# Optimization experiments

Hardware: AMD Instinct MI355X
Metric: run time of the kernel (lower is better)

Reference implementation:

```python
import jax, jax.numpy as jnp
import numpy as np

D_MODEL = 1024
N_HEADS = 16
D_HEAD = D_MODEL // N_HEADS  # 64
NEG_INF = -1e10


def setup_inputs() -> dict:
    key = jax.random.key(0)
    ks = jax.random.split(key, 12)
    B, Q, N = 2, 2048, 2048
    s = 1.0 / np.sqrt(D_MODEL)
    return {
        "q": jax.random.normal(ks[0], (B, Q, D_MODEL), jnp.float32),
        "k": jax.random.normal(ks[1], (B, N, D_MODEL), jnp.float32),
        "v": jax.random.normal(ks[2], (B, N, D_MODEL), jnp.float32),
        "mask": jax.random.randint(ks[3], (B, Q, N), 0, 2, jnp.int32),
        "Wq": jax.random.normal(ks[4], (D_MODEL, D_MODEL), jnp.float32) * s,
        "bq": jnp.zeros((D_MODEL,), jnp.float32),
        "Wk": jax.random.normal(ks[5], (D_MODEL, D_MODEL), jnp.float32) * s,
        "bk": jnp.zeros((D_MODEL,), jnp.float32),
        "Wv": jax.random.normal(ks[6], (D_MODEL, D_MODEL), jnp.float32) * s,
        "bv": jnp.zeros((D_MODEL,), jnp.float32),
        "Wo": jax.random.normal(ks[7], (D_MODEL, D_MODEL), jnp.float32) * s,
        "bo": jnp.zeros((D_MODEL,), jnp.float32),
    }


def reference(q, k, v, mask, Wq, bq, Wk, bk, Wv, bv, Wo, bo):
    B, Qlen, _ = q.shape
    N = k.shape[1]
    scale = 1.0 / np.sqrt(D_HEAD).astype(np.float32)
    # projections -> [B, S, H, Dh]
    qp = (q @ Wq + bq).reshape(B, Qlen, N_HEADS, D_HEAD)
    kp = (k @ Wk + bk).reshape(B, N, N_HEADS, D_HEAD)
    vp = (v @ Wv + bv).reshape(B, N, N_HEADS, D_HEAD)
    # scores [B, H, Q, N]
    score = jnp.einsum('bqhi,bnhi->bhqn', qp, kp) * scale
    score = jnp.where(mask[:, None, :, :] == 0, NEG_INF, score)
    attn_w = jax.nn.softmax(score, axis=-1)
    # dropout p=0.0 -> identity
    attn_out = jnp.einsum('bhqn,bnhi->bqhi', attn_w, vp).reshape(B, Qlen, D_MODEL)
    out = attn_out @ Wo + bo
    return out, attn_w
```

## Files before the change

### kernel.cpp

```cpp
#include <hip/hip_runtime.h>
#include <hip/hip_bf16.h>

#define BB 2
#define SS 2048
#define DMODEL 1024
#define NH 16
#define DHEAD 64
#define NEGINF (-1e10f)

typedef __attribute__((ext_vector_type(8))) short short8;
typedef __attribute__((ext_vector_type(4))) short short4v;
typedef __attribute__((ext_vector_type(4))) float f32x4;
typedef __hip_bfloat16 bf16;

__device__ __forceinline__ bf16 tobf(float x){ return __float2bfloat16(x); }
__device__ __forceinline__ float tof(bf16 x){ return __bfloat162float(x); }

__device__ __forceinline__ void gl_lds16(const void* g, void* l){
  __builtin_amdgcn_global_load_lds(
      (const __attribute__((address_space(1))) unsigned int*)g,
      (__attribute__((address_space(3))) unsigned int*)l, 16, 0, 0);
}


__global__ __launch_bounds__(256) void k_a3(const float* __restrict__ X, bf16* __restrict__ X3){
  long i = ((long)blockIdx.x*256 + threadIdx.x)*4;
  long r = i >> 10; int k = (int)(i & 1023);
  float4 x = *(const float4*)(X + i);
  float xs[4] = {x.x, x.y, x.z, x.w};
  alignas(8) bf16 hb[4], lb[4];
  #pragma unroll
  for(int j=0;j<4;j++){ hb[j]=tobf(xs[j]); lb[j]=tobf(xs[j]-tof(hb[j])); }
  bf16* base = X3 + r*3072 + k;
  *(short4v*)(base)        = *(short4v*)hb;
  *(short4v*)(base + 1024) = *(short4v*)lb;
  *(short4v*)(base + 2048) = *(short4v*)hb;
}

__global__ __launch_bounds__(256) void k_vbf(const float* __restrict__ X, bf16* __restrict__ Y){
  long i = ((long)blockIdx.x*256 + threadIdx.x)*4;
  float4 x = *(const float4*)(X + i);
  alignas(8) bf16 b[4] = {tobf(x.x), tobf(x.y), tobf(x.z), tobf(x.w)};
  *(short4v*)(Y + i) = *(short4v*)b;
}

template<int MODE>
__global__ __launch_bounds__(256) void k_wt(const float* __restrict__ W, bf16* __restrict__ out){
  __shared__ float t[64][65];
  const int kb = blockIdx.y*64, nb = blockIdx.x*64;
  const int tid = threadIdx.x;
  const int r = tid>>2, cq = tid&3;
  #pragma unroll
  for(int i=0;i<4;i++){
    float4 x = *(const float4*)&W[(long)(kb+r)*1024 + nb + cq*16 + i*4];
    t[r][cq*16+i*4+0]=x.x; t[r][cq*16+i*4+1]=x.y; t[r][cq*16+i*4+2]=x.z; t[r][cq*16+i*4+3]=x.w;
  }
  __syncthreads();
  alignas(16) bf16 hb[16], lb[16];
  #pragma unroll
  for(int i=0;i<16;i++){
    float x = t[cq*16+i][r];
    hb[i] = tobf(x);
    lb[i] = tobf(x - tof(hb[i]));
  }
  if (MODE==0){
    bf16* o = out + (long)(nb+r)*1024 + kb + cq*16;
    ((short8*)o)[0] = ((short8*)hb)[0]; ((short8*)o)[1] = ((short8*)hb)[1];
  } else {
    bf16* o = out + (long)(nb+r)*3072 + kb + cq*16;
    ((short8*)(o))[0]        = ((short8*)hb)[0]; ((short8*)(o))[1]        = ((short8*)hb)[1];
    ((short8*)(o+1024))[0]   = ((short8*)hb)[0]; ((short8*)(o+1024))[1]   = ((short8*)hb)[1];
    ((short8*)(o+2048))[0]   = ((short8*)lb)[0]; ((short8*)(o+2048))[1]   = ((short8*)lb)[1];
  }
}

__global__ __launch_bounds__(256) void k_vt(const bf16* __restrict__ vp, bf16* __restrict__ vpt){
  __shared__ alignas(16) bf16 t[64][72];
  const int sb = blockIdx.x*64;
  const int bh = blockIdx.y, b = bh>>4, h = bh&15;
  const int tid = threadIdx.x;
  {
    const int r = tid>>2, cg = tid&3;
    const bf16* src = vp + (long)(b*SS + sb + r)*DMODEL + h*64 + cg*16;
    *(short8*)&t[r][cg*16]   = *(const short8*)(src);
    *(short8*)&t[r][cg*16+8] = *(const short8*)(src+8);
  }
  __syncthreads();
  {
    const int d = tid>>2, sg = tid&3;
    alignas(16) bf16 ob[16];
    #pragma unroll
    for(int i=0;i<16;i++) ob[i] = t[sg*16+i][d];
    bf16* dst = vpt + ((long)bh*DHEAD + d)*SS + sb + sg*16;
    ((short8*)dst)[0] = ((short8*)ob)[0]; ((short8*)dst)[1] = ((short8*)ob)[1];
  }
}

enum { EPI_F32BIAS=0, EPI_BF16=1, EPI_SCORES=2, EPI_SPL3A=3, EPI_SPL3B=4 };

template<int EPI>
__global__ __launch_bounds__(256)
void gemm128(const bf16* __restrict__ A, int lda, long sAz,
             const bf16* __restrict__ Bt, int ldb, long sBz,
             float* __restrict__ Cf, bf16* __restrict__ Cb,
             int ldc, long sCz,
             const float* __restrict__ bias,
             const int* __restrict__ mask,
             float scale, int K)
{
  __shared__ alignas(16) bf16 lds[2][2][128*32];
  const int tid = threadIdx.x, wid = tid>>6, lane = tid&63;
  const int wr = wid>>1, wc = wid&1;
  const long bz = blockIdx.z;
  const int rowB = blockIdx.y*128, colB = blockIdx.x*128;
  const bf16* Ab = A + bz*sAz;
  const bf16* Bb = Bt + bz*sBz;

  auto stage = [&](int buf, int kt){
    #pragma unroll
    for(int i=0;i<2;i++){
      const int r0 = wid*32 + i*16;
      const char* ga = (const char*)(Ab + (long)(rowB + r0 + (lane>>2))*lda + kt*32) + (lane&3)*16;
      gl_lds16(ga, (char*)&lds[buf][0][0] + r0*64);
      const char* gb = (const char*)(Bb + (long)(colB + r0 + (lane>>2))*ldb + kt*32) + (lane&3)*16;
      gl_lds16(gb, (char*)&lds[buf][1][0] + r0*64);
    }
  };

  f32x4 acc[4][4];
  #pragma unroll
  for(int m=0;m<4;m++){
    #pragma unroll
    for(int n=0;n<4;n++){ acc[m][n][0]=0.f; acc[m][n][1]=0.f; acc[m][n][2]=0.f; acc[m][n][3]=0.f; }
  }

  const int nk = K/32;
  stage(0,0);
  int cur=0;
  for(int kt=0; kt<nk; ++kt){
    __syncthreads();
    if (kt+1<nk) stage(cur^1, kt+1);
    const bf16* la = &lds[cur][0][0];
    const bf16* lb = &lds[cur][1][0];
    const int rr = lane&15, kq = (lane>>4)*8;
    short8 af[4], bg[4];
    #pragma unroll
    for(int m=0;m<4;m++) af[m] = *(const short8*)(la + (wr*64+m*16+rr)*32 + kq);
    #pragma unroll
    for(int n=0;n<4;n++) bg[n] = *(const short8*)(lb + (wc*64+n*16+rr)*32 + kq);
    #pragma unroll
    for(int m=0;m<4;m++){
      #pragma unroll
      for(int n=0;n<4;n++)
        acc[m][n] = __builtin_amdgcn_mfma_f32_16x16x32_bf16(af[m], bg[n], acc[m][n], 0,0,0);
    }
    cur ^= 1;
  }

  #pragma unroll
  for(int m=0;m<4;m++){
    #pragma unroll
    for(int n=0;n<4;n++){
      const int row0 = rowB + wr*64 + m*16 + ((lane>>4)<<2);
      const int col  = colB + wc*64 + n*16 + (lane&15);
      #pragma unroll
      for(int j=0;j<4;j++){
        const int row = row0 + j;
        float x = acc[m][n][j];
        if constexpr (EPI==EPI_F32BIAS){
          Cf[bz*sCz + (long)row*ldc + col] = x + bias[col];
        } else if constexpr (EPI==EPI_BF16){
          Cb[bz*sCz + (long)row*ldc + col] = tobf(x + bias[col]);
        } else if constexpr (EPI==EPI_SCORES){
          const int b = (int)(bz>>4);
          const float s = x*scale;
          const int mv = mask[((long)b*SS + row)*SS + col];
          Cf[bz*sCz + (long)row*ldc + col] = (mv==0) ? NEGINF : s;
        } else {
          const float s = x + bias[col];
          const int b = row>>11, sq = row&2047;
          const int h = col>>6,  d  = col&63;
          bf16 hi = tobf(s);
          bf16 lo = tobf(s - tof(hi));
          bf16* o = Cb + (((long)(b*NH+h)*SS + sq)*192);
          if constexpr (EPI==EPI_SPL3A){ o[d]=hi; o[64+d]=lo; o[128+d]=hi; }
          else                          { o[d]=hi; o[64+d]=hi; o[128+d]=lo; }
        }
      }
    }
  }
}

__global__ __launch_bounds__(256)
void gemm_pv(const float* __restrict__ P, const bf16* __restrict__ Vt, bf16* __restrict__ O)
{
  __shared__ alignas(16) bf16 lA[2][128*32];
  __shared__ alignas(16) bf16 lB[2][64*32];
  const int tid=threadIdx.x, wid=tid>>6, lane=tid&63;
  const long z = blockIdx.z;
  const int b = (int)(z>>4), h = (int)(z&15);
  const int rowB = blockIdx.y*128;
  const float* Pz = P + z*((long)SS*SS) + (long)rowB*SS;
  const bf16*  Vz = Vt + z*((long)DHEAD*SS);

  auto stageB = [&](int buf, int kt){
    const char* g = (const char*)(Vz + (long)(wid*16 + (lane>>2))*SS + kt*32) + (lane&3)*16;
    gl_lds16(g, (char*)&lB[buf][0] + wid*16*64);
  };
  const int ar = tid>>1, acg = tid&1;
  auto loadA = [&](int kt, float4* f){
    const float* src = Pz + (long)ar*SS + kt*32 + acg*16;
    #pragma unroll
    for(int i=0;i<4;i++) f[i] = *(const float4*)(src + i*4);
  };
  auto writeA = [&](int buf, const float4* f){
    alignas(16) bf16 tmp[16];
    #pragma unroll
    for(int i=0;i<4;i++){
      tmp[i*4+0]=tobf(f[i].x); tmp[i*4+1]=tobf(f[i].y);
      tmp[i*4+2]=tobf(f[i].z); tmp[i*4+3]=tobf(f[i].w);
    }
    short8* d = (short8*)(&lA[buf][ar*32 + acg*16]);
    d[0] = ((short8*)tmp)[0]; d[1] = ((short8*)tmp)[1];
  };

  f32x4 acc[2][4];
  #pragma unroll
  for(int m=0;m<2;m++){
    #pragma unroll
    for(int n=0;n<4;n++){ acc[m][n][0]=0.f; acc[m][n][1]=0.f; acc[m][n][2]=0.f; acc[m][n][3]=0.f; }
  }

  float4 fr[4];
  loadA(0, fr); stageB(0,0); writeA(0, fr);
  int cur=0;
  const int nk = SS/32;
  for(int kt=0; kt<nk; ++kt){
    __syncthreads();
    float4 fn[4];
    if (kt+1<nk){ stageB(cur^1, kt+1); loadA(kt+1, fn); }
    const int rr=lane&15, kq=(lane>>4)*8;
    short8 af[2], bg[4];
    #pragma unroll
    for(int m=0;m<2;m++) af[m] = *(const short8*)(&lA[cur][(wid*32+m*16+rr)*32 + kq]);
    #pragma unroll
    for(int n=0;n<4;n++) bg[n] = *(const short8*)(&lB[cur][(n*16+rr)*32 + kq]);
    #pragma unroll
    for(int m=0;m<2;m++){
      #pragma unroll
      for(int n=0;n<4;n++)
        acc[m][n] = __builtin_amdgcn_mfma_f32_16x16x32_bf16(af[m], bg[n], acc[m][n], 0,0,0);
    }
    if (kt+1<nk) writeA(cur^1, fn);
    cur ^= 1;
  }

  #pragma unroll
  for(int m=0;m<2;m++){
    #pragma unroll
    for(int n=0;n<4;n++){
      const int row0 = rowB + wid*32 + m*16 + ((lane>>4)<<2);
      const int col  = n*16 + (lane&15);
      #pragma unroll
      for(int j=0;j<4;j++){
        const int row = row0 + j;
        O[((long)(b*SS + row))*DMODEL + h*64 + col] = tobf(acc[m][n][j]);
      }
    }
  }
}

__global__ __launch_bounds__(256) void k_softmax(float* __restrict__ attn){
  const long row = (long)blockIdx.x*4 + (threadIdx.x>>6);
  const int lane = threadIdx.x & 63;
  float* p = attn + row*SS;
  float v[32];
  float mx = -3.0e38f;
  #pragma unroll
  for(int i=0;i<8;i++){
    float4 t = *(const float4*)(p + i*256 + lane*4);
    v[i*4+0]=t.x; v[i*4+1]=t.y; v[i*4+2]=t.z; v[i*4+3]=t.w;
    mx = fmaxf(mx, fmaxf(fmaxf(t.x,t.y), fmaxf(t.z,t.w)));
  }
  #pragma unroll
  for(int off=32; off; off>>=1) mx = fmaxf(mx, __shfl_xor(mx, off));
  float sum = 0.f;
  #pragma unroll
  for(int i=0;i<32;i++){ v[i] = __expf(v[i]-mx); sum += v[i]; }
  #pragma unroll
  for(int off=32; off; off>>=1) sum += __shfl_xor(sum, off);
  const float inv = 1.0f/sum;
  #pragma unroll
  for(int i=0;i<8;i++){
    float4 t = { v[i*4+0]*inv, v[i*4+1]*inv, v[i*4+2]*inv, v[i*4+3]*inv };
    *(float4*)(p + i*256 + lane*4) = t;
  }
}

extern "C" void kernel_launch(void* const* d_in, const int* in_sizes, int n_in,
                              void* d_out, int out_size, void* d_ws, size_t ws_size,
                              hipStream_t stream) {
  const float* q    = (const float*)d_in[0];
  const float* k    = (const float*)d_in[1];
  const float* v    = (const float*)d_in[2];
  const int*   mask = (const int*)  d_in[3];
  const float* Wq   = (const float*)d_in[4];
  const float* bq   = (const float*)d_in[5];
  const float* Wk   = (const float*)d_in[6];
  const float* bk   = (const float*)d_in[7];
  const float* Wv   = (const float*)d_in[8];
  const float* bv   = (const float*)d_in[9];
  const float* Wo   = (const float*)d_in[10];
  const float* bo   = (const float*)d_in[11];

  float* out  = (float*)d_out;
  float* attn = out + (long)BB*SS*DMODEL;

  char* ws = (char*)d_ws;
  size_t o = 0;
  bf16* A3q = (bf16*)(ws+o); o += (size_t)4096*3072*2;
  bf16* A3k = (bf16*)(ws+o); o += (size_t)4096*3072*2;
  bf16* vbf = (bf16*)(ws+o); o += (size_t)4096*1024*2;
  bf16* Wq3 = (bf16*)(ws+o); o += (size_t)1024*3072*2;
  bf16* Wk3 = (bf16*)(ws+o); o += (size_t)1024*3072*2;
  bf16* Wvt = (bf16*)(ws+o); o += (size_t)1024*1024*2;
  bf16* Wot = (bf16*)(ws+o); o += (size_t)1024*1024*2;
  bf16* q3  = (bf16*)(ws+o); o += (size_t)32*2048*192*2;
  bf16* k3  = (bf16*)(ws+o); o += (size_t)32*2048*192*2;
  bf16* vpb = (bf16*)(ws+o); o += (size_t)4096*1024*2;
  bf16* vpt = (bf16*)(ws+o); o += (size_t)32*64*2048*2;
  bf16* abf = (bf16*)(ws+o); o += (size_t)4096*1024*2;

  dim3 blk(256);
  k_a3 <<<4096, blk, 0, stream>>>(q, A3q);
  k_a3 <<<4096, blk, 0, stream>>>(k, A3k);
  k_vbf<<<4096, blk, 0, stream>>>(v, vbf);
  k_wt<1><<<dim3(16,16), blk, 0, stream>>>(Wq, Wq3);
  k_wt<1><<<dim3(16,16), blk, 0, stream>>>(Wk, Wk3);
  k_wt<0><<<dim3(16,16), blk, 0, stream>>>(Wv, Wvt);
  k_wt<0><<<dim3(16,16), blk, 0, stream>>>(Wo, Wot);
  gemm128<EPI_SPL3A><<<dim3(8,32,1), blk, 0, stream>>>(A3q,3072,0, Wq3,3072,0, nullptr,q3, 0,0, bq, nullptr, 0.f, 3072);
  gemm128<EPI_SPL3B><<<dim3(8,32,1), blk, 0, stream>>>(A3k,3072,0, Wk3,3072,0, nullptr,k3, 0,0, bk, nullptr, 0.f, 3072);
  gemm128<EPI_BF16 ><<<dim3(8,32,1), blk, 0, stream>>>(vbf,1024,0, Wvt,1024,0, nullptr,vpb, 1024,0, bv, nullptr, 0.f, 1024);
  k_vt<<<dim3(32,32), blk, 0, stream>>>(vpb, vpt);
  gemm128<EPI_SCORES><<<dim3(16,16,32), blk, 0, stream>>>(
      q3,192,(long)SS*192, k3,192,(long)SS*192, attn,nullptr, SS,(long)SS*SS,
      nullptr, mask, 0.125f, 192);
  k_softmax<<<(BB*NH*SS)/4, blk, 0, stream>>>(attn);
  gemm_pv<<<dim3(1,16,32), blk, 0, stream>>>(attn, vpt, abf);
  gemm128<EPI_F32BIAS><<<dim3(8,32,1), blk, 0, stream>>>(abf,1024,0, Wot,1024,0, out,nullptr, 1024,0, bo, nullptr, 0.f, 1024);
}
```

Baseline: 1.284 ms.

## Fuse softmax into scores and PV kernels with fp16 scores and bitpacked mask

```diff
diff --git a/kernel.cpp b/kernel.cpp
--- a/kernel.cpp
+++ b/kernel.cpp
@@ -1,5 +1,6 @@
 #include <hip/hip_runtime.h>
 #include <hip/hip_bf16.h>
+#include <hip/hip_fp16.h>
 
 #define BB 2
 #define SS 2048
@@ -7,6 +8,7 @@
 #define NH 16
 #define DHEAD 64
 #define NEGINF (-1e10f)
+#define MASKF16 (-65504.0f)
 
 typedef __attribute__((ext_vector_type(8))) short short8;
 typedef __attribute__((ext_vector_type(4))) short short4v;
@@ -22,6 +24,14 @@
       (__attribute__((address_space(3))) unsigned int*)l, 16, 0, 0);
 }
 
+
+__global__ __launch_bounds__(256) void k_maskbits(const int* __restrict__ mask,
+                                                  unsigned long long* __restrict__ bits){
+  long t = (long)blockIdx.x*256 + threadIdx.x;
+  int m = mask[t];
+  unsigned long long bal = __ballot(m != 0);
+  if ((threadIdx.x & 63) == 0) bits[t>>6] = bal;
+}
 
 __global__ __launch_bounds__(256) void k_a3(const float* __restrict__ X, bf16* __restrict__ X3){
   long i = ((long)blockIdx.x*256 + threadIdx.x)*4;
@@ -96,7 +106,7 @@
   }
 }
 
-enum { EPI_F32BIAS=0, EPI_BF16=1, EPI_SCORES=2, EPI_SPL3A=3, EPI_SPL3B=4 };
+enum { EPI_F32BIAS=0, EPI_BF16=1, EPI_SPL3A=3, EPI_SPL3B=4 };
 
 template<int EPI>
 __global__ __launch_bounds__(256)
@@ -105,8 +115,7 @@
              float* __restrict__ Cf, bf16* __restrict__ Cb,
              int ldc, long sCz,
              const float* __restrict__ bias,
-             const int* __restrict__ mask,
-             float scale, int K)
+             int K)
 {
   __shared__ alignas(16) bf16 lds[2][2][128*32];
   const int tid = threadIdx.x, wid = tid>>6, lane = tid&63;
@@ -171,11 +180,6 @@
           Cf[bz*sCz + (long)row*ldc + col] = x + bias[col];
         } else if constexpr (EPI==EPI_BF16){
           Cb[bz*sCz + (long)row*ldc + col] = tobf(x + bias[col]);
-        } else if constexpr (EPI==EPI_SCORES){
-          const int b = (int)(bz>>4);
-          const float s = x*scale;
-          const int mv = mask[((long)b*SS + row)*SS + col];
-          Cf[bz*sCz + (long)row*ldc + col] = (mv==0) ? NEGINF : s;
         } else {
           const float s = x + bias[col];
           const int b = row>>11, sq = row&2047;
@@ -192,7 +196,114 @@
 }
 
 __global__ __launch_bounds__(256)
-void gemm_pv(const float* __restrict__ P, const bf16* __restrict__ Vt, bf16* __restrict__ O)
+void gemm_scores(const bf16* __restrict__ A, const bf16* __restrict__ Bt,
+                 const unsigned int* __restrict__ bits,
+                 __half* __restrict__ Sf, float2* __restrict__ partials, float scale)
+{
+  __shared__ alignas(16) bf16 lds[2][2][128*32];
+  __shared__ unsigned int bitlds[128][4];
+  const int tid = threadIdx.x, wid = tid>>6, lane = tid&63;
+  const int wr = wid>>1, wc = wid&1;
+  const long z = blockIdx.z;
+  const int b = (int)(z>>4);
+  const int rowB = blockIdx.y*128, colB = blockIdx.x*128;
+  const bf16* Ab = A + z*((long)SS*192);
+  const bf16* Bb = Bt + z*((long)SS*192);
+
+  auto stage = [&](int buf, int kt){
+    #pragma unroll
+    for(int i=0;i<2;i++){
+      const int r0 = wid*32 + i*16;
+      const char* ga = (const char*)(Ab + (long)(rowB + r0 + (lane>>2))*192 + kt*32) + (lane&3)*16;
+      gl_lds16(ga, (char*)&lds[buf][0][0] + r0*64);
+      const char* gb = (const char*)(Bb + (long)(colB + r0 + (lane>>2))*192 + kt*32) + (lane&3)*16;
+      gl_lds16(gb, (char*)&lds[buf][1][0] + r0*64);
+    }
+  };
+
+  f32x4 acc[4][4];
+  #pragma unroll
+  for(int m=0;m<4;m++){
+    #pragma unroll
+    for(int n=0;n<4;n++){ acc[m][n][0]=0.f; acc[m][n][1]=0.f; acc[m][n][2]=0.f; acc[m][n][3]=0.f; }
+  }
+
+  stage(0,0);
+  int cur=0;
+  for(int kt=0; kt<6; ++kt){
+    __syncthreads();
+    if (kt+1<6) stage(cur^1, kt+1);
+    const bf16* la = &lds[cur][0][0];
+    const bf16* lb = &lds[cur][1][0];
+    const int rr = lane&15, kq = (lane>>4)*8;
+    short8 af[4], bg[4];
+    #pragma unroll
+    for(int m=0;m<4;m++) af[m] = *(const short8*)(la + (wr*64+m*16+rr)*32 + kq);
+    #pragma unroll
+    for(int n=0;n<4;n++) bg[n] = *(const short8*)(lb + (wc*64+n*16+rr)*32 + kq);
+    #pragma unroll
+    for(int m=0;m<4;m++){
+      #pragma unroll
+      for(int n=0;n<4;n++)
+        acc[m][n] = __builtin_amdgcn_mfma_f32_16x16x32_bf16(af[m], bg[n], acc[m][n], 0,0,0);
+    }
+    cur ^= 1;
+  }
+
+  if (tid < 128){
+    *(uint4*)&bitlds[tid][0] =
+        *(const uint4*)(bits + ((long)(b*SS + rowB + tid))*64 + (colB>>5));
+  }
+  __syncthreads();
+
+  __half* Sz = Sf + z*((long)SS*SS);
+  #pragma unroll
+  for(int m=0;m<4;m++){
+    #pragma unroll
+    for(int j=0;j<4;j++){
+      const int row_l = wr*64 + m*16 + ((lane>>4)<<2) + j;
+      const long rowOff = (long)(rowB + row_l)*SS;
+      float x[4];
+      #pragma unroll
+      for(int n=0;n<4;n++){
+        const int col_l = wc*64 + n*16 + (lane&15);
+        const unsigned w = bitlds[row_l][col_l>>5];
+        const bool keep = (w >> (col_l&31)) & 1u;
+        const float s = keep ? acc[m][n][j]*scale : MASKF16;
+        const __half hh = __float2half(s);
+        Sz[rowOff + colB + col_l] = hh;
+        x[n] = __half2float(hh);
+      }
+      float mx = fmaxf(fmaxf(x[0],x[1]), fmaxf(x[2],x[3]));
+      #pragma unroll
+      for(int off=1; off<16; off<<=1) mx = fmaxf(mx, __shfl_xor(mx, off));
+      float sm = __expf(x[0]-mx)+__expf(x[1]-mx)+__expf(x[2]-mx)+__expf(x[3]-mx);
+      #pragma unroll
+      for(int off=1; off<16; off<<=1) sm += __shfl_xor(sm, off);
+      if ((lane&15)==0)
+        partials[((long)z*SS + rowB + row_l)*32 + blockIdx.x*2 + wc] = make_float2(mx, sm);
+    }
+  }
+}
+
+__global__ __launch_bounds__(256) void k_stats(const float2* __restrict__ partials,
+                                               float2* __restrict__ stats){
+  const long row = (long)blockIdx.x*4 + (threadIdx.x>>6);
+  const int lane = threadIdx.x & 63;
+  float2 pr = make_float2(-3.0e38f, 0.f);
+  if (lane < 32) pr = partials[row*32 + lane];
+  float M = pr.x;
+  #pragma unroll
+  for(int off=32; off; off>>=1) M = fmaxf(M, __shfl_xor(M, off));
+  float v = (lane < 32) ? pr.y * __expf(pr.x - M) : 0.f;
+  #pragma unroll
+  for(int off=32; off; off>>=1) v += __shfl_xor(v, off);
+  if (lane == 0) stats[row] = make_float2(M, 1.0f / v);
+}
+
+__global__ __launch_bounds__(256)
+void gemm_pv(const __half* __restrict__ S, const float2* __restrict__ stats,
+             const bf16* __restrict__ Vt, float* __restrict__ attnw, bf16* __restrict__ O)
 {
   __shared__ alignas(16) bf16 lA[2][128*32];
   __shared__ alignas(16) bf16 lB[2][64*32];
@@ -200,7 +311,8 @@
   const long z = blockIdx.z;
   const int b = (int)(z>>4), h = (int)(z&15);
   const int rowB = blockIdx.y*128;
-  const float* Pz = P + z*((long)SS*SS) + (long)rowB*SS;
+  const __half* Sz = S + z*((long)SS*SS) + (long)rowB*SS;
+  float*       Wz = attnw + z*((long)SS*SS) + (long)rowB*SS;
   const bf16*  Vz = Vt + z*((long)DHEAD*SS);
 
   auto stageB = [&](int buf, int kt){
@@ -208,18 +320,24 @@
     gl_lds16(g, (char*)&lB[buf][0] + wid*16*64);
   };
   const int ar = tid>>1, acg = tid&1;
-  auto loadA = [&](int kt, float4* f){
-    const float* src = Pz + (long)ar*SS + kt*32 + acg*16;
-    #pragma unroll
-    for(int i=0;i<4;i++) f[i] = *(const float4*)(src + i*4);
+  const float2 st = stats[z*SS + rowB + ar];
+  const float M = st.x, invZ = st.y;
+
+  auto loadA = [&](int kt, short8* r){
+    const short8* src = (const short8*)(Sz + (long)ar*SS + kt*32 + acg*16);
+    r[0] = src[0]; r[1] = src[1];
   };
-  auto writeA = [&](int buf, const float4* f){
+  auto procA = [&](int buf, int kt, const short8* r){
+    const __half* hp = (const __half*)r;
+    alignas(16) float p[16];
+    #pragma unroll
+    for(int i=0;i<16;i++) p[i] = __expf(__half2float(hp[i]) - M) * invZ;
+    float* w = Wz + (long)ar*SS + kt*32 + acg*16;
+    #pragma unroll
+    for(int i=0;i<4;i++) *(float4*)(w + i*4) = *(float4*)&p[i*4];
     alignas(16) bf16 tmp[16];
     #pragma unroll
-    for(int i=0;i<4;i++){
-      tmp[i*4+0]=tobf(f[i].x); tmp[i*4+1]=tobf(f[i].y);
-      tmp[i*4+2]=tobf(f[i].z); tmp[i*4+3]=tobf(f[i].w);
-    }
+    for(int i=0;i<16;i++) tmp[i] = tobf(p[i]);
     short8* d = (short8*)(&lA[buf][ar*32 + acg*16]);
     d[0] = ((short8*)tmp)[0]; d[1] = ((short8*)tmp)[1];
   };
@@ -231,13 +349,13 @@
     for(int n=0;n<4;n++){ acc[m][n][0]=0.f; acc[m][n][1]=0.f; acc[m][n][2]=0.f; acc[m][n][3]=0.f; }
   }
 
-  float4 fr[4];
-  loadA(0, fr); stageB(0,0); writeA(0, fr);
+  short8 fr[2];
+  loadA(0, fr); stageB(0,0); procA(0, 0, fr);
   int cur=0;
   const int nk = SS/32;
   for(int kt=0; kt<nk; ++kt){
     __syncthreads();
-    float4 fn[4];
+    short8 fn[2];
     if (kt+1<nk){ stageB(cur^1, kt+1); loadA(kt+1, fn); }
     const int rr=lane&15, kq=(lane>>4)*8;
     short8 af[2], bg[4];
@@ -251,7 +369,7 @@
       for(int n=0;n<4;n++)
         acc[m][n] = __builtin_amdgcn_mfma_f32_16x16x32_bf16(af[m], bg[n], acc[m][n], 0,0,0);
     }
-    if (kt+1<nk) writeA(cur^1, fn);
+    if (kt+1<nk) procA(cur^1, kt+1, fn);
     cur ^= 1;
   }
 
@@ -267,33 +385,6 @@
         O[((long)(b*SS + row))*DMODEL + h*64 + col] = tobf(acc[m][n][j]);
       }
     }
-  }
-}
-
-__global__ __launch_bounds__(256) void k_softmax(float* __restrict__ attn){
-  const long row = (long)blockIdx.x*4 + (threadIdx.x>>6);
-  const int lane = threadIdx.x & 63;
-  float* p = attn + row*SS;
-  float v[32];
-  float mx = -3.0e38f;
-  #pragma unroll
-  for(int i=0;i<8;i++){
-    float4 t = *(const float4*)(p + i*256 + lane*4);
-    v[i*4+0]=t.x; v[i*4+1]=t.y; v[i*4+2]=t.z; v[i*4+3]=t.w;
-    mx = fmaxf(mx, fmaxf(fmaxf(t.x,t.y), fmaxf(t.z,t.w)));
-  }
-  #pragma unroll
-  for(int off=32; off; off>>=1) mx = fmaxf(mx, __shfl_xor(mx, off));
-  float sum = 0.f;
-  #pragma unroll
-  for(int i=0;i<32;i++){ v[i] = __expf(v[i]-mx); sum += v[i]; }
-  #pragma unroll
-  for(int off=32; off; off>>=1) sum += __shfl_xor(sum, off);
-  const float inv = 1.0f/sum;
-  #pragma unroll
-  for(int i=0;i<8;i++){
-    float4 t = { v[i*4+0]*inv, v[i*4+1]*inv, v[i*4+2]*inv, v[i*4+3]*inv };
-    *(float4*)(p + i*256 + lane*4) = t;
   }
 }
 
@@ -330,8 +421,13 @@
   bf16* vpb = (bf16*)(ws+o); o += (size_t)4096*1024*2;
   bf16* vpt = (bf16*)(ws+o); o += (size_t)32*64*2048*2;
   bf16* abf = (bf16*)(ws+o); o += (size_t)4096*1024*2;
+  unsigned long long* bits = (unsigned long long*)(ws+o); o += (size_t)BB*SS*32*8;
+  __half* scoresF = (__half*)(ws+o); o += (size_t)32*SS*SS*2;
+  float2* partials = (float2*)(ws+o); o += (size_t)32*SS*32*8;
+  float2* stats   = (float2*)(ws+o); o += (size_t)32*SS*8;
 
   dim3 blk(256);
+  k_maskbits<<<(BB*SS*SS)/256, blk, 0, stream>>>(mask, bits);
   k_a3 <<<4096, blk, 0, stream>>>(q, A3q);
   k_a3 <<<4096, blk, 0, stream>>>(k, A3k);
   k_vbf<<<4096, blk, 0, stream>>>(v, vbf);
@@ -339,14 +435,13 @@
   k_wt<1><<<dim3(16,16), blk, 0, stream>>>(Wk, Wk3);
   k_wt<0><<<dim3(16,16), blk, 0, stream>>>(Wv, Wvt);
   k_wt<0><<<dim3(16,16), blk, 0, stream>>>(Wo, Wot);
-  gemm128<EPI_SPL3A><<<dim3(8,32,1), blk, 0, stream>>>(A3q,3072,0, Wq3,3072,0, nullptr,q3, 0,0, bq, nullptr, 0.f, 3072);
-  gemm128<EPI_SPL3B><<<dim3(8,32,1), blk, 0, stream>>>(A3k,3072,0, Wk3,3072,0, nullptr,k3, 0,0, bk, nullptr, 0.f, 3072);
-  gemm128<EPI_BF16 ><<<dim3(8,32,1), blk, 0, stream>>>(vbf,1024,0, Wvt,1024,0, nullptr,vpb, 1024,0, bv, nullptr, 0.f, 1024);
+  gemm128<EPI_SPL3A><<<dim3(8,32,1), blk, 0, stream>>>(A3q,3072,0, Wq3,3072,0, nullptr,q3, 0,0, bq, 3072);
+  gemm128<EPI_SPL3B><<<dim3(8,32,1), blk, 0, stream>>>(A3k,3072,0, Wk3,3072,0, nullptr,k3, 0,0, bk, 3072);
+  gemm128<EPI_BF16 ><<<dim3(8,32,1), blk, 0, stream>>>(vbf,1024,0, Wvt,1024,0, nullptr,vpb, 1024,0, bv, 1024);
   k_vt<<<dim3(32,32), blk, 0, stream>>>(vpb, vpt);
-  gemm128<EPI_SCORES><<<dim3(16,16,32), blk, 0, stream>>>(
-      q3,192,(long)SS*192, k3,192,(long)SS*192, attn,nullptr, SS,(long)SS*SS,
-      nullptr, mask, 0.125f, 192);
-  k_softmax<<<(BB*NH*SS)/4, blk, 0, stream>>>(attn);
-  gemm_pv<<<dim3(1,16,32), blk, 0, stream>>>(attn, vpt, abf);
-  gemm128<EPI_F32BIAS><<<dim3(8,32,1), blk, 0, stream>>>(abf,1024,0, Wot,1024,0, out,nullptr, 1024,0, bo, nullptr, 0.f, 1024);
-}
+  gemm_scores<<<dim3(16,16,32), blk, 0, stream>>>(q3, k3, (const unsigned int*)bits,
+                                                  scoresF, partials, 0.125f);
+  k_stats<<<(32*SS)/4, blk, 0, stream>>>(partials, stats);
+  gemm_pv<<<dim3(1,16,32), blk, 0, stream>>>(scoresF, stats, vpt, attn, abf);
+  gemm128<EPI_F32BIAS><<<dim3(8,32,1), blk, 0, stream>>>(abf,1024,0, Wot,1024,0, out,nullptr, 1024,0, bo, 1024);
+}
```

New measurement: 1.100 ms. -14.4%, faster.
